# Kernel tuning notes

Hardware: AMD Instinct MI355X
Metric: run time of the kernel (lower is better)

## Reference

```python
import jax, jax.numpy as jnp
from jax import lax
import numpy as np

N = 10000      # num_nodes
T = 24         # hist_len
IN_DIM = 16
HID = 128
HEADS = 4
E = 160000     # num_edges
PRED = 24
NEG_SLOPE = 0.2  # GATv2 LeakyReLU default


def _lstm_layer(xs, wih, whh, bih, bhh):
    # xs: [T, N, D]; PyTorch gate order i, f, g, o
    Hh = whh.shape[1]
    h0 = jnp.zeros((xs.shape[1], Hh), xs.dtype)
    def step(carry, xt):
        h, c = carry
        g = xt @ wih.T + bih + h @ whh.T + bhh
        i, f, gg, o = jnp.split(g, 4, axis=-1)
        c = jax.nn.sigmoid(f) * c + jax.nn.sigmoid(i) * jnp.tanh(gg)
        h = jax.nn.sigmoid(o) * jnp.tanh(c)
        return (h, c), h
    (_, _), out = lax.scan(step, (h0, h0), xs)
    return out  # [T, N, Hh]


def _gatv2(z, src, dst, wl, bl, wr, br, att, bias):
    # PyG GATv2Conv: share_weights=False, concat=True, add_self_loops=False
    n = z.shape[0]
    xl = (z @ wl.T + bl).reshape(n, HEADS, HID)   # source/message transform
    xr = (z @ wr.T + br).reshape(n, HEADS, HID)   # target transform
    e = jax.nn.leaky_relu(xl[src] + xr[dst], NEG_SLOPE)   # [E, H, C]
    score = jnp.einsum('ehc,hc->eh', e, att)              # [E, H]
    smax = jax.ops.segment_max(score, dst, num_segments=n)
    p = jnp.exp(score - smax[dst])
    denom = jax.ops.segment_sum(p, dst, num_segments=n)
    alpha = p / (denom[dst] + 1e-16)                      # segment softmax over in-edges
    out = jax.ops.segment_sum(xl[src] * alpha[:, :, None], dst, num_segments=n)
    return out.reshape(n, HEADS * HID) + bias


def setup_inputs() -> dict:
    key = jax.random.key(0)
    ks = iter(jax.random.split(key, 64))
    def W(shape):
        return jax.random.normal(next(ks), shape, jnp.float32) / np.sqrt(shape[-1])
    inp = {}
    inp['x'] = jax.random.normal(next(ks), (N, T, IN_DIM), jnp.float32)
    inp['edge_index'] = jax.random.randint(next(ks), (2, E), 0, N, jnp.int32)
    inp['mlp_in_w0'] = W((HID, IN_DIM)); inp['mlp_in_b0'] = jnp.zeros((HID,), jnp.float32)
    inp['mlp_in_w1'] = W((HID, HID));    inp['mlp_in_b1'] = jnp.zeros((HID,), jnp.float32)
    for l in range(2):  # nn.LSTM(num_layers = lstm_num_layers*2 = 2)
        inp[f'lstm_wih{l}'] = W((4 * HID, HID))
        inp[f'lstm_whh{l}'] = W((4 * HID, HID))
        inp[f'lstm_bih{l}'] = jnp.zeros((4 * HID,), jnp.float32)
        inp[f'lstm_bhh{l}'] = jnp.zeros((4 * HID,), jnp.float32)
    for l in range(2):  # nGAT_layer = 2
        inp[f'gat{l}_wl'] = W((HEADS * HID, HID))
        inp[f'gat{l}_bl'] = jnp.zeros((HEADS * HID,), jnp.float32)
        inp[f'gat{l}_wr'] = W((HEADS * HID, HID))
        inp[f'gat{l}_br'] = jnp.zeros((HEADS * HID,), jnp.float32)
        inp[f'gat{l}_att'] = W((HEADS, HID))
        inp[f'gat{l}_bias'] = jnp.zeros((HEADS * HID,), jnp.float32)
        inp[f'gat{l}_pw'] = W((HID, HEADS * HID))
        inp[f'gat{l}_pb'] = jnp.zeros((HID,), jnp.float32)
    inp['mlp_out_w0'] = W((HID, HID));  inp['mlp_out_b0'] = jnp.zeros((HID,), jnp.float32)
    inp['mlp_out_w1'] = W((PRED, HID)); inp['mlp_out_b1'] = jnp.zeros((PRED,), jnp.float32)
    return inp


def _forward(x, edge_index, mlp_in_w0, mlp_in_b0, mlp_in_w1, mlp_in_b1,
             lstm_wih0, lstm_whh0, lstm_bih0, lstm_bhh0,
             lstm_wih1, lstm_whh1, lstm_bih1, lstm_bhh1,
             gat0_wl, gat0_bl, gat0_wr, gat0_br, gat0_att, gat0_bias, gat0_pw, gat0_pb,
             gat1_wl, gat1_bl, gat1_wr, gat1_br, gat1_att, gat1_bias, gat1_pw, gat1_pb,
             mlp_out_w0, mlp_out_b0, mlp_out_w1, mlp_out_b1):
    src, dst = edge_index[0], edge_index[1]
    h = jnp.transpose(x, (1, 0, 2))                       # [T, N, in_dim]
    # MLP_layers_in: Linear(in,hid), Linear(hid,hid), ReLU
    h = h @ mlp_in_w0.T + mlp_in_b0
    h = jax.nn.relu(h @ mlp_in_w1.T + mlp_in_b1)
    # 2-layer unidirectional LSTM
    h = _lstm_layer(h, lstm_wih0, lstm_whh0, lstm_bih0, lstm_bhh0)
    h = _lstm_layer(h, lstm_wih1, lstm_whh1, lstm_bih1, lstm_bhh1)
    z = h[-1]                                             # [N, HID] last timestep
    # GAT block x2: GATv2Conv -> Linear(heads*hid, hid) -> ReLU
    z = _gatv2(z, src, dst, gat0_wl, gat0_bl, gat0_wr, gat0_br, gat0_att, gat0_bias)
    z = jax.nn.relu(z @ gat0_pw.T + gat0_pb)
    z = _gatv2(z, src, dst, gat1_wl, gat1_bl, gat1_wr, gat1_br, gat1_att, gat1_bias)
    z = jax.nn.relu(z @ gat1_pw.T + gat1_pb)
    # MLP_layers_out: Linear(hid,hid), ReLU, Linear(hid, pred_len)
    z = jax.nn.relu(z @ mlp_out_w0.T + mlp_out_b0)
    return z @ mlp_out_w1.T + mlp_out_b1                  # [N, PRED]


def reference(x, edge_index, mlp_in_w0, mlp_in_b0, mlp_in_w1, mlp_in_b1,
              lstm_wih0, lstm_whh0, lstm_bih0, lstm_bhh0,
              lstm_wih1, lstm_whh1, lstm_bih1, lstm_bhh1,
              gat0_wl, gat0_bl, gat0_wr, gat0_br, gat0_att, gat0_bias, gat0_pw, gat0_pb,
              gat1_wl, gat1_bl, gat1_wr, gat1_br, gat1_att, gat1_bias, gat1_pw, gat1_pb,
              mlp_out_w0, mlp_out_b0, mlp_out_w1, mlp_out_b1):
    return _forward(x, edge_index, mlp_in_w0, mlp_in_b0, mlp_in_w1, mlp_in_b1,
                    lstm_wih0, lstm_whh0, lstm_bih0, lstm_bhh0,
                    lstm_wih1, lstm_whh1, lstm_bih1, lstm_bhh1,
                    gat0_wl, gat0_bl, gat0_wr, gat0_br, gat0_att, gat0_bias, gat0_pw, gat0_pb,
                    gat1_wl, gat1_bl, gat1_wr, gat1_br, gat1_att, gat1_bias, gat1_pw, gat1_pb,
                    mlp_out_w0, mlp_out_b0, mlp_out_w1, mlp_out_b1)
```

## Files before the change

kernel.cpp:

```cpp
#include <hip/hip_runtime.h>
#include <hip/hip_bf16.h>

#define NNODES 10000
#define TLEN 24
#define INDIM 16
#define HID 128
#define GDIM 512

typedef __hip_bfloat16 bf16;
typedef short v8s __attribute__((ext_vector_type(8)));
typedef float v4f __attribute__((ext_vector_type(4)));

__device__ inline float u2f(unsigned u){ return __uint_as_float(u); }
__device__ inline float frcp(float x){ return __builtin_amdgcn_rcpf(x); }

__device__ inline void unpack8(uint4 v, float* f){
  f[0]=u2f(v.x<<16); f[1]=u2f(v.x&0xFFFF0000u);
  f[2]=u2f(v.y<<16); f[3]=u2f(v.y&0xFFFF0000u);
  f[4]=u2f(v.z<<16); f[5]=u2f(v.z&0xFFFF0000u);
  f[6]=u2f(v.w<<16); f[7]=u2f(v.w&0xFFFF0000u);
}

__global__ __launch_bounds__(256) void conv_w_k(
    const float* s0, const float* s1, const float* s2, const float* s3,
    const float* s4, const float* s5, const float* s6, const float* s7,
    const float* s8, const float* s9, const float* s10,
    bf16* __restrict__ dst, int* __restrict__ deg)
{
  int idx = blockIdx.x*256 + threadIdx.x;
  if (idx < NNODES) deg[idx] = 0;
  if (idx >= 671744) return;
  int b = blockIdx.x >> 8;
  const float* s;
  if      (b == 0) s = s0;
  else if (b == 1) s = s1;
  else if (b == 2) s = s2;
  else if (b == 3) s = s3;
  else if (b == 4) s = s4;
  else if (b == 5) s = s5;
  else if (b == 6) s = s6;
  else if (b == 7) s = s7;
  else if (b == 8) s = s8;
  else if (b == 9) s = s9;
  else             s = s10;
  dst[idx] = __float2bfloat16(s[idx - b*65536]);
}

__global__ __launch_bounds__(256) void prep_w_k(
    const float* __restrict__ miw0, const float* __restrict__ mib0,
    const float* __restrict__ miw1, const float* __restrict__ mib1,
    const float* __restrict__ bih0, const float* __restrict__ bhh0,
    const float* __restrict__ bih1, const float* __restrict__ bhh1,
    const float* __restrict__ bl0, const float* __restrict__ br0,
    const float* __restrict__ bl1, const float* __restrict__ br1,
    float* __restrict__ Wp, float* __restrict__ bp,
    float* __restrict__ bsum, float* __restrict__ gblr,
    const int* __restrict__ dst, int* __restrict__ deg, int E)
{
  int t = threadIdx.x;
  int b = blockIdx.x;
  if (b >= 9){
    int e = (b-9)*256 + t;
    if (e < E){
      unsigned d = (unsigned)dst[e];
      if (d < (unsigned)NNODES) atomicAdd(&deg[d], 1);
    }
    return;
  }
  if (b < 8){
    int idx = b*256 + t;
    int j = idx >> 4, d = idx & 15;
    float s = 0.f;
    for (int k=0;k<HID;k++) s += miw1[j*HID+k] * miw0[k*INDIM+d];
    Wp[idx] = s;
    return;
  }
  if (t < HID){
    float s = mib1[t];
    for (int k=0;k<HID;k++) s += miw1[t*HID+k] * mib0[k];
    bp[t] = s;
  }
  for (int i = t; i < GDIM; i += 256){
    bsum[i]        = bih0[i] + bhh0[i];
    bsum[GDIM + i] = bih1[i] + bhh1[i];
  }
  for (int i = t; i < GDIM; i += 256){
    gblr[i]          = bl0[i];
    gblr[GDIM + i]   = br0[i];
    gblr[1024 + i]   = bl1[i];
    gblr[1536 + i]   = br1[i];
  }
}

__global__ __launch_bounds__(1024) void scan_k(
    const int* __restrict__ deg, int* __restrict__ offs,
    int* __restrict__ cursor, int n)
{
  __shared__ int wsum[16];
  __shared__ int wpre[16];
  const int t = threadIdx.x;
  const int lane = t & 63, wv = t >> 6;
  const int lo = t*10;
  int loc[10];
  int s = 0;
  #pragma unroll
  for (int i=0;i<10;i++){
    int idx = lo + i;
    int d = (idx < n) ? deg[idx] : 0;
    loc[i] = d; s += d;
  }
  int sc = s;
  #pragma unroll
  for (int off=1; off<64; off<<=1){
    int u = __shfl_up(sc, off);
    if (lane >= off) sc += u;
  }
  if (lane == 63) wsum[wv] = sc;
  __syncthreads();
  if (t == 0){
    int run = 0;
    #pragma unroll
    for (int i=0;i<16;i++){ wpre[i] = run; run += wsum[i]; }
    offs[n] = run;
  }
  __syncthreads();
  int run = wpre[wv] + (sc - s);
  #pragma unroll
  for (int i=0;i<10;i++){
    int idx = lo + i;
    if (idx < n){ offs[idx] = run; cursor[idx] = run; run += loc[i]; }
  }
}

__global__ __launch_bounds__(256) void mlp_in_k(
    const float* __restrict__ x, const float* __restrict__ Wp,
    const float* __restrict__ bp, bf16* __restrict__ X0,
    const int* __restrict__ srcp, const int* __restrict__ dstp,
    int* __restrict__ curs, int* __restrict__ srcs, int E)
{
  __shared__ __align__(16) float xs[64*16];
  const int tid = threadIdx.x;
  const int m0 = blockIdx.x*64;
  {
    int row = tid >> 2, q = tid & 3;
    int m = m0 + row;
    int t = m / NNODES, n = m - t*NNODES;
    float4 v = *(const float4*)(x + ((size_t)n*TLEN + t)*INDIM + q*4);
    *(float4*)(xs + row*16 + q*4) = v;
  }
  {
    int gid = blockIdx.x*256 + tid;
    if (gid < E){
      unsigned d = (unsigned)dstp[gid];
      if (d < (unsigned)NNODES){
        int p = atomicAdd(&curs[d], 1);
        unsigned s = (unsigned)srcp[gid];
        srcs[p] = (s < (unsigned)NNODES) ? (int)s : 0;
      }
    }
  }
  const int j = tid & 127;
  const int half = tid >> 7;
  const float* wr = Wp + j*INDIM;
  float4 w0 = *(const float4*)(wr);
  float4 w1 = *(const float4*)(wr + 4);
  float4 w2 = *(const float4*)(wr + 8);
  float4 w3 = *(const float4*)(wr + 12);
  float bj = bp[j];
  __syncthreads();
  #pragma unroll 4
  for (int mi=0; mi<32; mi++){
    int row = mi*2 + half;
    const float* xr = xs + row*16;
    float4 a0 = *(const float4*)(xr);
    float4 a1 = *(const float4*)(xr + 4);
    float4 a2 = *(const float4*)(xr + 8);
    float4 a3 = *(const float4*)(xr + 12);
    float s = bj
      + a0.x*w0.x + a0.y*w0.y + a0.z*w0.z + a0.w*w0.w
      + a1.x*w1.x + a1.y*w1.y + a1.z*w1.z + a1.w*w1.w
      + a2.x*w2.x + a2.y*w2.y + a2.z*w2.z + a2.w*w2.w
      + a3.x*w3.x + a3.y*w3.y + a3.z*w3.z + a3.w*w3.w;
    s = s > 0.f ? s : 0.f;
    X0[(size_t)(m0+row)*HID + j] = __float2bfloat16(s);
  }
}

template<int WRITE_ALL>
__device__ __forceinline__ void lstm_layer(
    bf16* Xio, const bf16* __restrict__ Wih, const bf16* __restrict__ Whh,
    const float* __restrict__ bias, bf16* __restrict__ out,
    bf16* hs, bf16* xs, int m0)
{
  const int tid = threadIdx.x;
  const int lane = tid & 63, w = tid >> 6;
  const int r16 = lane & 15, quad = lane >> 4;
  const int HB = 48*136;

  v8s wbi[4][4], wbh[4][4];
  #pragma unroll
  for (int g=0; g<4; g++)
    #pragma unroll
    for (int kc=0; kc<4; kc++){
      size_t o = (size_t)(g*HID + w*16 + r16)*HID + kc*32 + quad*8;
      wbi[g][kc] = *(const v8s*)(Wih + o);
      wbh[g][kc] = *(const v8s*)(Whh + o);
    }
  float bg[4];
  #pragma unroll
  for (int g=0; g<4; g++) bg[g] = bias[g*HID + w*16 + r16];

  const int row0 = tid >> 4;
  const int c8   = (tid & 15) * 8;
  const int row1 = 32 + (tid >> 4);
  const int gr0 = m0 + row0;
  const int gr1 = m0 + row1;
  const int gr0c = gr0 < NNODES ? gr0 : NNODES-1;
  const int gr1c = gr1 < NNODES ? gr1 : NNODES-1;
  const bf16* ldp0 = Xio + (size_t)gr0c*HID + c8;
  const bf16* ldp1 = Xio + (size_t)gr1c*HID + c8;
  bf16* stp0 = Xio + (size_t)gr0*HID + c8;
  bf16* stp1 = Xio + (size_t)gr1*HID + c8;
  const size_t TS = (size_t)NNODES*HID;

  for (int i = tid; i < 816; i += 512)
    *(uint4*)((char*)hs + i*16) = make_uint4(0,0,0,0);

  {
    uint4 a = *(const uint4*)ldp0;
    *(uint4*)(xs + row0*136 + c8) = a;
    if (tid < 256){
      uint4 b = *(const uint4*)ldp1;
      *(uint4*)(xs + row1*136 + c8) = b;
    }
  }
  __syncthreads();

  float c[3][4];
  #pragma unroll
  for (int tl=0; tl<3; tl++)
    #pragma unroll
    for (int r=0; r<4; r++) c[tl][r] = 0.f;

  const int fb = r16*136 + quad*8;

  #pragma unroll 1
  for (int t=0; t<TLEN; t++){
    const int cur = t & 1, nxt = cur ^ 1;
    const bf16* xrd = xs + cur*HB;
    const bf16* hrd = hs + cur*HB;
    bf16* hwr = hs + nxt*HB;

    const int tn = (t+1 < TLEN) ? t+1 : TLEN-1;
    uint4 xa = *(const uint4*)(ldp0 + (size_t)tn*TS);
    uint4 xb;
    if (tid < 256) xb = *(const uint4*)(ldp1 + (size_t)tn*TS);

    #pragma unroll
    for (int tl=0; tl<3; tl++){
      v4f acc[4];
      #pragma unroll
      for (int g=0; g<4; g++) acc[g] = (v4f)0.f;

      #pragma unroll
      for (int kc=0; kc<4; kc++){
        v8s av = *(const v8s*)(xrd + tl*2176 + fb + kc*32);
        #pragma unroll
        for (int g=0; g<4; g++)
          acc[g] = __builtin_amdgcn_mfma_f32_16x16x32_bf16(av, wbi[g][kc], acc[g], 0, 0, 0);
      }
      #pragma unroll
      for (int kc=0; kc<4; kc++){
        v8s hv = *(const v8s*)(hrd + tl*2176 + fb + kc*32);
        #pragma unroll
        for (int g=0; g<4; g++)
          acc[g] = __builtin_amdgcn_mfma_f32_16x16x32_bf16(hv, wbh[g][kc], acc[g], 0, 0, 0);
      }

      #pragma unroll
      for (int r=0; r<4; r++){
        float iv = acc[0][r] + bg[0];
        float fv = acc[1][r] + bg[1];
        float gv = acc[2][r] + bg[2];
        float ov = acc[3][r] + bg[3];
        float sf = frcp(1.f + __expf(-fv));
        float ei = __expf(-iv);
        float tg = __expf(-2.f*fabsf(gv));
        float itg = copysignf((1.f - tg)*frcp((1.f + ei)*(1.f + tg)), gv);
        float cn = sf*c[tl][r] + itg;
        c[tl][r] = cn;
        float eo = __expf(-ov);
        float tc = __expf(-2.f*fabsf(cn));
        float hh = copysignf((1.f - tc)*frcp((1.f + eo)*(1.f + tc)), cn);
        hwr[(tl*16 + quad*4 + r)*136 + w*16 + r16] = __float2bfloat16(hh);
      }
    }

    *(uint4*)(xs + nxt*HB + row0*136 + c8) = xa;
    if (tid < 256) *(uint4*)(xs + nxt*HB + row1*136 + c8) = xb;

    __syncthreads();

    if (WRITE_ALL){
      uint4 h0 = *(const uint4*)(hwr + row0*136 + c8);
      if (gr0 < NNODES) *(uint4*)(stp0 + (size_t)t*TS) = h0;
      if (tid < 256){
        uint4 h1v = *(const uint4*)(hwr + row1*136 + c8);
        if (gr1 < NNODES) *(uint4*)(stp1 + (size_t)t*TS) = h1v;
      }
    }
  }

  if (!WRITE_ALL){
    const bf16* hf = hs + (TLEN & 1)*HB;
    uint4 h0 = *(const uint4*)(hf + row0*136 + c8);
    if (gr0 < NNODES) *(uint4*)(out + (size_t)gr0*HID + c8) = h0;
    if (tid < 256){
      uint4 h1v = *(const uint4*)(hf + row1*136 + c8);
      if (gr1 < NNODES) *(uint4*)(out + (size_t)gr1*HID + c8) = h1v;
    }
  }
}

__global__ __launch_bounds__(512) void lstm_f2(
    bf16* X0, const bf16* __restrict__ wih0, const bf16* __restrict__ whh0,
    const bf16* __restrict__ wih1, const bf16* __restrict__ whh1,
    const float* __restrict__ bsum, bf16* __restrict__ zf)
{
  __shared__ __align__(16) bf16 hs[2][48*136];
  __shared__ __align__(16) bf16 xs[2][48*136];
  const int m0 = blockIdx.x*48;
  lstm_layer<1>(X0, wih0, whh0, bsum,        nullptr, &hs[0][0], &xs[0][0], m0);
  __syncthreads();
  lstm_layer<0>(X0, wih1, whh1, bsum + GDIM, zf,      &hs[0][0], &xs[0][0], m0);
}

template<int ACT>
__global__ __launch_bounds__(256) void gemm_bt(
    const bf16* __restrict__ A, const bf16* __restrict__ B,
    const float* __restrict__ bias, bf16* __restrict__ C,
    int M, int N, int K)
{
  __shared__ __align__(16) bf16 As[128*40];
  __shared__ __align__(16) bf16 Bs[128*40];
  const int tid = threadIdx.x;
  const int m0 = blockIdx.x*128, n0 = blockIdx.y*128;
  const int lane = tid & 63, wave = tid >> 6;
  const int r16 = lane & 15, quad = lane >> 4;

  v4f acc[2][8];
  #pragma unroll
  for (int a=0;a<2;a++)
    #pragma unroll
    for (int b=0;b<8;b++) acc[a][b] = (v4f)0.f;

  for (int k0=0; k0<K; k0+=32){
    #pragma unroll
    for (int i=0;i<2;i++){
      int li = tid + i*256;
      int row = li >> 2, q4 = li & 3;
      uint4 va = make_uint4(0,0,0,0);
      int gm = m0 + row;
      if (gm < M) va = *(const uint4*)(A + (size_t)gm*K + k0 + q4*8);
      *(uint4*)(As + row*40 + q4*8) = va;
      uint4 vb = make_uint4(0,0,0,0);
      int gn = n0 + row;
      if (gn < N) vb = *(const uint4*)(B + (size_t)gn*K + k0 + q4*8);
      *(uint4*)(Bs + row*40 + q4*8) = vb;
    }
    __syncthreads();
    v8s av[2], bv[8];
    #pragma unroll
    for (int mi=0;mi<2;mi++)
      av[mi] = *(const v8s*)(As + (wave*32 + mi*16 + r16)*40 + quad*8);
    #pragma unroll
    for (int ni=0;ni<8;ni++)
      bv[ni] = *(const v8s*)(Bs + (ni*16 + r16)*40 + quad*8);
    #pragma unroll
    for (int mi=0;mi<2;mi++)
      #pragma unroll
      for (int ni=0;ni<8;ni++)
        acc[mi][ni] = __builtin_amdgcn_mfma_f32_16x16x32_bf16(av[mi], bv[ni], acc[mi][ni], 0, 0, 0);
    __syncthreads();
  }

  #pragma unroll
  for (int mi=0;mi<2;mi++){
    #pragma unroll
    for (int r=0;r<4;r++){
      int row = m0 + wave*32 + mi*16 + quad*4 + r;
      if (row >= M) continue;
      #pragma unroll
      for (int ni=0;ni<8;ni++){
        int col = n0 + ni*16 + r16;
        float v = acc[mi][ni][r] + bias[col];
        if (ACT == 1) v = v > 0.f ? v : 0.f;
        C[(size_t)row*N + col] = __float2bfloat16(v);
      }
    }
  }
}

template<int ACT>
__global__ __launch_bounds__(256) void gemm_bt64(
    const bf16* __restrict__ A, const bf16* __restrict__ B,
    const float* __restrict__ bias, bf16* __restrict__ C,
    int M, int K)
{
  __shared__ __align__(16) bf16 As[64*40];
  __shared__ __align__(16) bf16 Bs[128*40];
  const int tid = threadIdx.x;
  const int m0 = blockIdx.x*64;
  const int lane = tid & 63, wave = tid >> 6;
  const int r16 = lane & 15, quad = lane >> 4;

  v4f acc[8];
  #pragma unroll
  for (int b=0;b<8;b++) acc[b] = (v4f)0.f;

  for (int k0=0; k0<K; k0+=32){
    {
      int row = tid >> 2, q4 = tid & 3;
      uint4 va = make_uint4(0,0,0,0);
      int gm = m0 + row;
      if (gm < M) va = *(const uint4*)(A + (size_t)gm*K + k0 + q4*8);
      *(uint4*)(As + row*40 + q4*8) = va;
    }
    #pragma unroll
    for (int i=0;i<2;i++){
      int li = tid + i*256;
      int row = li >> 2, q4 = li & 3;
      uint4 vb = *(const uint4*)(B + (size_t)row*K + k0 + q4*8);
      *(uint4*)(Bs + row*40 + q4*8) = vb;
    }
    __syncthreads();
    v8s av, bv[8];
    av = *(const v8s*)(As + (wave*16 + r16)*40 + quad*8);
    #pragma unroll
    for (int ni=0;ni<8;ni++)
      bv[ni] = *(const v8s*)(Bs + (ni*16 + r16)*40 + quad*8);
    #pragma unroll
    for (int ni=0;ni<8;ni++)
      acc[ni] = __builtin_amdgcn_mfma_f32_16x16x32_bf16(av, bv[ni], acc[ni], 0, 0, 0);
    __syncthreads();
  }

  #pragma unroll
  for (int r=0;r<4;r++){
    int row = m0 + wave*16 + quad*4 + r;
    if (row >= M) continue;
    #pragma unroll
    for (int ni=0;ni<8;ni++){
      int col = ni*16 + r16;
      float v = acc[ni][r] + bias[col];
      if (ACT == 1) v = v > 0.f ? v : 0.f;
      C[(size_t)row*HID + col] = __float2bfloat16(v);
    }
  }
}

__global__ __launch_bounds__(256) void mlp_out_fused_k(
    const bf16* __restrict__ A, const bf16* __restrict__ B,
    const float* __restrict__ bias, const float* __restrict__ w1,
    const float* __restrict__ b1, float* __restrict__ out, int M)
{
  __shared__ __align__(16) bf16 As[64*40];
  __shared__ __align__(16) bf16 Bs[128*40];
  __shared__ __align__(16) bf16 o0s[64*136];
  const int tid = threadIdx.x;
  const int m0 = blockIdx.x*64;
  const int lane = tid & 63, wave = tid >> 6;
  const int r16 = lane & 15, quad = lane >> 4;

  v4f acc[8];
  #pragma unroll
  for (int b=0;b<8;b++) acc[b] = (v4f)0.f;

  for (int k0=0; k0<HID; k0+=32){
    {
      int row = tid >> 2, q4 = tid & 3;
      uint4 va = make_uint4(0,0,0,0);
      int gm = m0 + row;
      if (gm < M) va = *(const uint4*)(A + (size_t)gm*HID + k0 + q4*8);
      *(uint4*)(As + row*40 + q4*8) = va;
    }
    #pragma unroll
    for (int i=0;i<2;i++){
      int li = tid + i*256;
      int row = li >> 2, q4 = li & 3;
      uint4 vb = *(const uint4*)(B + (size_t)row*HID + k0 + q4*8);
      *(uint4*)(Bs + row*40 + q4*8) = vb;
    }
    __syncthreads();
    v8s av, bv[8];
    av = *(const v8s*)(As + (wave*16 + r16)*40 + quad*8);
    #pragma unroll
    for (int ni=0;ni<8;ni++)
      bv[ni] = *(const v8s*)(Bs + (ni*16 + r16)*40 + quad*8);
    #pragma unroll
    for (int ni=0;ni<8;ni++)
      acc[ni] = __builtin_amdgcn_mfma_f32_16x16x32_bf16(av, bv[ni], acc[ni], 0, 0, 0);
    __syncthreads();
  }

  #pragma unroll
  for (int r=0;r<4;r++){
    int row = wave*16 + quad*4 + r;
    #pragma unroll
    for (int ni=0;ni<8;ni++){
      int col = ni*16 + r16;
      float v = acc[ni][r] + bias[col];
      v = v > 0.f ? v : 0.f;
      o0s[row*136 + col] = __float2bfloat16(v);
    }
  }
  __syncthreads();

  for (int idx = tid; idx < 64*24; idx += 256){
    int row = idx / 24, j = idx - row*24;
    if (m0 + row >= M) continue;
    const bf16* ar = o0s + row*136;
    const float* wr = w1 + j*HID;
    float s = b1[j];
    for (int k=0;k<HID;k+=8){
      float fa[8];
      unpack8(*(const uint4*)(ar+k), fa);
      float4 w0 = *(const float4*)(wr + k);
      float4 w1v = *(const float4*)(wr + k + 4);
      s += fa[0]*w0.x + fa[1]*w0.y + fa[2]*w0.z + fa[3]*w0.w
         + fa[4]*w1v.x + fa[5]*w1v.y + fa[6]*w1v.z + fa[7]*w1v.w;
    }
    out[(size_t)(m0+row)*24 + j] = s;
  }
}

__global__ __launch_bounds__(256) void gat_onl(
    const int* __restrict__ offs, const int* __restrict__ srcs,
    const bf16* __restrict__ xc, const float* __restrict__ att,
    const float* __restrict__ gbias, bf16* __restrict__ agg)
{
  int d = blockIdx.x*4 + (threadIdx.x >> 6);
  if (d >= NNODES) return;
  int lane = threadIdx.x & 63;
  float fr[8];
  unpack8(*(const uint4*)(xc + (size_t)d*1024 + 512 + lane*8), fr);
  float4 a0 = *(const float4*)(att + lane*8);
  float4 a1 = *(const float4*)(att + lane*8 + 4);
  float fa[8] = {a0.x,a0.y,a0.z,a0.w,a1.x,a1.y,a1.z,a1.w};
  int i0 = offs[d], i1 = offs[d+1];

  float m = -3.4e38f, den = 0.f;
  float acc[8] = {0,0,0,0,0,0,0,0};

  if (i0 < i1){
    uint4 r0 = *(const uint4*)(xc + (size_t)srcs[i0]*1024 + lane*8);
    uint4 r1 = r0;
    if (i0+1 < i1) r1 = *(const uint4*)(xc + (size_t)srcs[i0+1]*1024 + lane*8);
    for (int i=i0; i<i1; i++){
      uint4 r2 = r1;
      if (i+2 < i1) r2 = *(const uint4*)(xc + (size_t)srcs[i+2]*1024 + lane*8);
      float fl[8];
      unpack8(r0, fl);
      float p = 0.f;
      #pragma unroll
      for (int q=0;q<8;q++){
        float v = fl[q] + fr[q];
        v = v > 0.f ? v : 0.2f*v;
        p += v*fa[q];
      }
      p += __shfl_xor(p, 1); p += __shfl_xor(p, 2);
      p += __shfl_xor(p, 4); p += __shfl_xor(p, 8);
      float mn = fmaxf(m, p);
      float corr = __expf(m - mn);
      float w = __expf(p - mn);
      den = den*corr + w;
      #pragma unroll
      for (int q=0;q<8;q++) acc[q] = acc[q]*corr + w*fl[q];
      m = mn;
      r0 = r1; r1 = r2;
    }
  }
  float r = 1.f/(den + 1e-16f);
  float4 b0 = *(const float4*)(gbias + lane*8);
  float4 b1 = *(const float4*)(gbias + lane*8 + 4);
  float fb[8] = {b0.x,b0.y,b0.z,b0.w,b1.x,b1.y,b1.z,b1.w};
  #pragma unroll
  for (int q=0;q<8;q++)
    agg[(size_t)d*GDIM + lane*8 + q] = __float2bfloat16(acc[q]*r + fb[q]);
}


extern "C" void kernel_launch(void* const* d_in, const int* in_sizes, int n_in,
                              void* d_out, int out_size, void* d_ws, size_t ws_size,
                              hipStream_t stream)
{
  const float* x   = (const float*)d_in[0];
  const int*   ei  = (const int*)d_in[1];
  const int E = in_sizes[1] / 2;
  const int* srcp = ei;
  const int* dstp = ei + E;

  const float* miw0 = (const float*)d_in[2];
  const float* mib0 = (const float*)d_in[3];
  const float* miw1 = (const float*)d_in[4];
  const float* mib1 = (const float*)d_in[5];
  const float* wih0 = (const float*)d_in[6];
  const float* whh0 = (const float*)d_in[7];
  const float* bih0 = (const float*)d_in[8];
  const float* bhh0 = (const float*)d_in[9];
  const float* wih1 = (const float*)d_in[10];
  const float* whh1 = (const float*)d_in[11];
  const float* bih1 = (const float*)d_in[12];
  const float* bhh1 = (const float*)d_in[13];
  const float* g_wl[2]   = {(const float*)d_in[14], (const float*)d_in[22]};
  const float* g_bl[2]   = {(const float*)d_in[15], (const float*)d_in[23]};
  const float* g_wr[2]   = {(const float*)d_in[16], (const float*)d_in[24]};
  const float* g_br[2]   = {(const float*)d_in[17], (const float*)d_in[25]};
  const float* g_att[2]  = {(const float*)d_in[18], (const float*)d_in[26]};
  const float* g_bias[2] = {(const float*)d_in[19], (const float*)d_in[27]};
  const float* g_pw[2]   = {(const float*)d_in[20], (const float*)d_in[28]};
  const float* g_pb[2]   = {(const float*)d_in[21], (const float*)d_in[29]};
  const float* mow0 = (const float*)d_in[30];
  const float* mob0 = (const float*)d_in[31];
  const float* mow1 = (const float*)d_in[32];
  const float* mob1 = (const float*)d_in[33];
  (void)n_in; (void)out_size; (void)ws_size;

  char* base = (char*)d_ws;
  size_t off = 0;
  auto carve = [&](size_t n)->char*{
    char* p = base + off;
    off = (off + n + 255) & ~(size_t)255;
    return p;
  };
  char*  X0r = carve((size_t)TLEN*NNODES*HID*2);
  bf16*  zf  = (bf16*)carve((size_t)NNODES*HID*2);
  float* Wp  = (float*)carve(HID*INDIM*4);
  float* bp  = (float*)carve(HID*4);
  float* bsum= (float*)carve(2*GDIM*4);
  float* gblr= (float*)carve(2*1024*4);
  bf16*  wbf = (bf16*)carve((size_t)671744*2);
  int*   offsb = (int*)carve((size_t)(NNODES+1)*4);
  int*   curs  = (int*)carve((size_t)NNODES*4);
  int*   srcs  = (int*)carve((size_t)E*4);
  int*   deg   = (int*)carve((size_t)NNODES*4);
  bf16*  agg   = (bf16*)carve((size_t)NNODES*GDIM*2);

  const bf16* wih0b = wbf + 0;
  const bf16* whh0b = wbf + 65536;
  const bf16* wih1b = wbf + 131072;
  const bf16* whh1b = wbf + 196608;
  const bf16* wlr0b = wbf + 262144;
  const bf16* pw0b  = wbf + 393216;
  const bf16* wlr1b = wbf + 458752;
  const bf16* pw1b  = wbf + 589824;
  const bf16* mow0b = wbf + 655360;
  const bf16* wlrb[2] = {wlr0b, wlr1b};
  const bf16* pwb[2]  = {pw0b, pw1b};

  bf16* X0 = (bf16*)X0r;
  bf16* xc = (bf16*)X0r;
  bf16* z2 = (bf16*)(X0r + 20480000);
  bf16* z3 = (bf16*)(X0r + 23040000);

  conv_w_k<<<2624, 256, 0, stream>>>(wih0, whh0, wih1, whh1,
                                     g_wl[0], g_wr[0], g_pw[0],
                                     g_wl[1], g_wr[1], g_pw[1], mow0, wbf, deg);
  prep_w_k<<<9 + (E+255)/256, 256, 0, stream>>>(miw0, mib0, miw1, mib1,
                                  bih0, bhh0, bih1, bhh1,
                                  g_bl[0], g_br[0], g_bl[1], g_br[1],
                                  Wp, bp, bsum, gblr, dstp, deg, E);
  scan_k<<<1, 1024, 0, stream>>>(deg, offsb, curs, NNODES);

  mlp_in_k<<<(TLEN*NNODES)/64, 256, 0, stream>>>(x, Wp, bp, X0,
                                                 srcp, dstp, curs, srcs, E);

  const int NBL48 = (NNODES + 47) / 48;
  lstm_f2<<<NBL48, 512, 0, stream>>>(X0, wih0b, whh0b, wih1b, whh1b, bsum, zf);

  const bf16* zin = zf;
  bf16* zouts[2] = {z2, z3};
  const int NB64 = (NNODES + 63) / 64;
  for (int l=0; l<2; l++){
    gemm_bt<0><<<dim3(79,8), 256, 0, stream>>>(zin, wlrb[l], gblr + l*1024, xc, NNODES, 1024, HID);
    gat_onl<<<(NNODES+3)/4, 256, 0, stream>>>(offsb, srcs, xc, g_att[l], g_bias[l], agg);
    gemm_bt64<1><<<NB64, 256, 0, stream>>>(agg, pwb[l], g_pb[l], zouts[l], NNODES, GDIM);
    zin = zouts[l];
  }

  mlp_out_fused_k<<<NB64, 256, 0, stream>>>(z3, mow0b, mob0, mow1, mob1,
                                            (float*)d_out, NNODES);
}
```

Measured before the change: 501.2 us.

## Fuse input MLP and edge CSR fill into the LSTM kernel prologue

```diff
diff --git a/kernel.cpp b/kernel.cpp
--- a/kernel.cpp
+++ b/kernel.cpp
@@ -132,60 +132,6 @@
   }
 }
 
-__global__ __launch_bounds__(256) void mlp_in_k(
-    const float* __restrict__ x, const float* __restrict__ Wp,
-    const float* __restrict__ bp, bf16* __restrict__ X0,
-    const int* __restrict__ srcp, const int* __restrict__ dstp,
-    int* __restrict__ curs, int* __restrict__ srcs, int E)
-{
-  __shared__ __align__(16) float xs[64*16];
-  const int tid = threadIdx.x;
-  const int m0 = blockIdx.x*64;
-  {
-    int row = tid >> 2, q = tid & 3;
-    int m = m0 + row;
-    int t = m / NNODES, n = m - t*NNODES;
-    float4 v = *(const float4*)(x + ((size_t)n*TLEN + t)*INDIM + q*4);
-    *(float4*)(xs + row*16 + q*4) = v;
-  }
-  {
-    int gid = blockIdx.x*256 + tid;
-    if (gid < E){
-      unsigned d = (unsigned)dstp[gid];
-      if (d < (unsigned)NNODES){
-        int p = atomicAdd(&curs[d], 1);
-        unsigned s = (unsigned)srcp[gid];
-        srcs[p] = (s < (unsigned)NNODES) ? (int)s : 0;
-      }
-    }
-  }
-  const int j = tid & 127;
-  const int half = tid >> 7;
-  const float* wr = Wp + j*INDIM;
-  float4 w0 = *(const float4*)(wr);
-  float4 w1 = *(const float4*)(wr + 4);
-  float4 w2 = *(const float4*)(wr + 8);
-  float4 w3 = *(const float4*)(wr + 12);
-  float bj = bp[j];
-  __syncthreads();
-  #pragma unroll 4
-  for (int mi=0; mi<32; mi++){
-    int row = mi*2 + half;
-    const float* xr = xs + row*16;
-    float4 a0 = *(const float4*)(xr);
-    float4 a1 = *(const float4*)(xr + 4);
-    float4 a2 = *(const float4*)(xr + 8);
-    float4 a3 = *(const float4*)(xr + 12);
-    float s = bj
-      + a0.x*w0.x + a0.y*w0.y + a0.z*w0.z + a0.w*w0.w
-      + a1.x*w1.x + a1.y*w1.y + a1.z*w1.z + a1.w*w1.w
-      + a2.x*w2.x + a2.y*w2.y + a2.z*w2.z + a2.w*w2.w
-      + a3.x*w3.x + a3.y*w3.y + a3.z*w3.z + a3.w*w3.w;
-    s = s > 0.f ? s : 0.f;
-    X0[(size_t)(m0+row)*HID + j] = __float2bfloat16(s);
-  }
-}
-
 template<int WRITE_ALL>
 __device__ __forceinline__ void lstm_layer(
     bf16* Xio, const bf16* __restrict__ Wih, const bf16* __restrict__ Whh,
@@ -325,11 +271,79 @@
 __global__ __launch_bounds__(512) void lstm_f2(
     bf16* X0, const bf16* __restrict__ wih0, const bf16* __restrict__ whh0,
     const bf16* __restrict__ wih1, const bf16* __restrict__ whh1,
-    const float* __restrict__ bsum, bf16* __restrict__ zf)
+    const float* __restrict__ bsum, bf16* __restrict__ zf,
+    const float* __restrict__ x, const float* __restrict__ Wp,
+    const float* __restrict__ bp,
+    const int* __restrict__ srcp, const int* __restrict__ dstp,
+    int* __restrict__ curs, int* __restrict__ srcs, int E)
 {
   __shared__ __align__(16) bf16 hs[2][48*136];
   __shared__ __align__(16) bf16 xs[2][48*136];
+  const int tid = threadIdx.x;
   const int m0 = blockIdx.x*48;
+
+  {
+    for (int e = blockIdx.x*512 + tid; e < E; e += gridDim.x*512){
+      unsigned d = (unsigned)dstp[e];
+      if (d < (unsigned)NNODES){
+        int p = atomicAdd(&curs[d], 1);
+        unsigned sv = (unsigned)srcp[e];
+        srcs[p] = (sv < (unsigned)NNODES) ? (int)sv : 0;
+      }
+    }
+
+    float* xrow = (float*)&hs[0][0];
+    const int j  = tid & 127;
+    const int rq = tid >> 7;
+    const float* wr = Wp + j*INDIM;
+    float4 w0 = *(const float4*)(wr);
+    float4 w1 = *(const float4*)(wr + 4);
+    float4 w2 = *(const float4*)(wr + 8);
+    float4 w3 = *(const float4*)(wr + 12);
+    float bj = bp[j];
+
+    if (tid < 192){
+      int r = tid >> 2, kq = tid & 3;
+      int n = m0 + r; if (n >= NNODES) n = NNODES-1;
+      *(float4*)(xrow + r*16 + kq*4) =
+          *(const float4*)(x + ((size_t)n*TLEN + 0)*INDIM + kq*4);
+    }
+    __syncthreads();
+
+    for (int t=0; t<TLEN; t++){
+      const int cur = t & 1, nxt = cur ^ 1;
+      float4 xa;
+      if (tid < 192 && t+1 < TLEN){
+        int r = tid >> 2, kq = tid & 3;
+        int n = m0 + r; if (n >= NNODES) n = NNODES-1;
+        xa = *(const float4*)(x + ((size_t)n*TLEN + (t+1))*INDIM + kq*4);
+      }
+      const float* xb = xrow + cur*768;
+      bf16* dst = X0 + (size_t)t*NNODES*HID;
+      #pragma unroll 2
+      for (int rr=0; rr<12; rr++){
+        int r = rq*12 + rr;
+        int n = m0 + r;
+        const float* a = xb + r*16;
+        float4 a0 = *(const float4*)(a);
+        float4 a1 = *(const float4*)(a + 4);
+        float4 a2 = *(const float4*)(a + 8);
+        float4 a3 = *(const float4*)(a + 12);
+        float s = bj
+          + a0.x*w0.x + a0.y*w0.y + a0.z*w0.z + a0.w*w0.w
+          + a1.x*w1.x + a1.y*w1.y + a1.z*w1.z + a1.w*w1.w
+          + a2.x*w2.x + a2.y*w2.y + a2.z*w2.z + a2.w*w2.w
+          + a3.x*w3.x + a3.y*w3.y + a3.z*w3.z + a3.w*w3.w;
+        s = s > 0.f ? s : 0.f;
+        if (n < NNODES) dst[(size_t)n*HID + j] = __float2bfloat16(s);
+      }
+      if (tid < 192 && t+1 < TLEN){
+        int r = tid >> 2, kq = tid & 3;
+        *(float4*)(xrow + nxt*768 + r*16 + kq*4) = xa;
+      }
+      __syncthreads();
+    }
+  }
   lstm_layer<1>(X0, wih0, whh0, bsum,        nullptr, &hs[0][0], &xs[0][0], m0);
   __syncthreads();
   lstm_layer<0>(X0, wih1, whh1, bsum + GDIM, zf,      &hs[0][0], &xs[0][0], m0);
@@ -672,11 +686,9 @@
                                   Wp, bp, bsum, gblr, dstp, deg, E);
   scan_k<<<1, 1024, 0, stream>>>(deg, offsb, curs, NNODES);
 
-  mlp_in_k<<<(TLEN*NNODES)/64, 256, 0, stream>>>(x, Wp, bp, X0,
-                                                 srcp, dstp, curs, srcs, E);
-
   const int NBL48 = (NNODES + 47) / 48;
-  lstm_f2<<<NBL48, 512, 0, stream>>>(X0, wih0b, whh0b, wih1b, whh1b, bsum, zf);
+  lstm_f2<<<NBL48, 512, 0, stream>>>(X0, wih0b, whh0b, wih1b, whh1b, bsum, zf,
+                                     x, Wp, bp, srcp, dstp, curs, srcs, E);
 
   const bf16* zin = zf;
   bf16* zouts[2] = {z2, z3};
```

After: 519.8 us. 1.04x slower.
